# Kernel tuning notes

Hardware: AMD Instinct MI355X
Metric: run time of the kernel (lower is better)

The kernel has to match this reference:

```python
import jax, jax.numpy as jnp
from jax import lax
import numpy as np

VOCAB, EMBED, HIDDEN, BATCH, MAXLEN = 32000, 512, 1024, 64, 64


def setup_inputs() -> dict:
    key = jax.random.key(0)
    ks = jax.random.split(key, 18)
    s = 0.02
    H, E, V = HIDDEN, EMBED, VOCAB
    return {
        "thought": jax.random.normal(ks[0], (BATCH, H), jnp.float32),
        "emb_table": jax.random.normal(ks[1], (V, E), jnp.float32) * s,
        "w_ih0": jax.random.normal(ks[2], (4 * H, E + H), jnp.float32) * s,
        "w_hh0": jax.random.normal(ks[3], (4 * H, H), jnp.float32) * s,
        "b_ih0": jax.random.normal(ks[4], (4 * H,), jnp.float32) * s,
        "b_hh0": jax.random.normal(ks[5], (4 * H,), jnp.float32) * s,
        "w_ih1": jax.random.normal(ks[6], (4 * H, H), jnp.float32) * s,
        "w_hh1": jax.random.normal(ks[7], (4 * H, H), jnp.float32) * s,
        "b_ih1": jax.random.normal(ks[8], (4 * H,), jnp.float32) * s,
        "b_hh1": jax.random.normal(ks[9], (4 * H,), jnp.float32) * s,
        "gw1": jax.random.normal(ks[10], (H, H), jnp.float32) * s,
        "gb1": jax.random.normal(ks[11], (H,), jnp.float32) * s,
        "gw2": jax.random.normal(ks[12], (1, H), jnp.float32) * s,
        "gb2": jax.random.normal(ks[13], (1,), jnp.float32) * s,
        "out_w": jax.random.normal(ks[14], (V, H), jnp.float32) * s,
        "out_b": jax.random.normal(ks[15], (V,), jnp.float32) * s,
        "max_len": MAXLEN,
    }


def lstm_cell(x, h, c, w_ih, w_hh, b_ih, b_hh):
    # torch nn.LSTM gate order: i, f, g, o
    g = x @ w_ih.T + b_ih + h @ w_hh.T + b_hh
    i, f, gg, o = jnp.split(g, 4, axis=-1)
    c2 = jax.nn.sigmoid(f) * c + jax.nn.sigmoid(i) * jnp.tanh(gg)
    return jax.nn.sigmoid(o) * jnp.tanh(c2), c2


def reference(thought, emb_table, w_ih0, w_hh0, b_ih0, b_hh0, w_ih1, w_hh1,
              b_ih1, b_hh1, gw1, gb1, gw2, gb2, out_w, out_b, max_len):
    """Generation branch of BioDecoder.forward (captions=None), eval mode, epoch=0."""
    B, H = thought.shape
    V = out_w.shape[0]
    temperature, top_p, top_k = 0.9, 0.88, 60
    key = jax.random.key(42)
    rows = jnp.arange(B)[:, None]

    def filt(logits):
        # top-k filter
        kth = lax.top_k(logits, top_k)[0][:, -1:]
        logits = jnp.where(logits < kth, -jnp.inf, logits)
        # nucleus (top-p) filter
        sl, si = lax.top_k(logits, V)  # full descending sort
        cum = jnp.cumsum(jax.nn.softmax(sl, axis=-1), axis=-1)
        rm = cum > top_p
        rm = jnp.concatenate([jnp.zeros_like(rm[:, :1]), rm[:, :-1]], axis=-1)  # always keep best
        mask = jnp.zeros_like(rm).at[rows, si].set(rm)
        return jnp.where(mask, -jnp.inf, logits)

    def step(carry, t):
        h1, c1, h2, c2, prev_ctx, word, counts, hist = carry
        x = jnp.concatenate([emb_table[word], prev_ctx], axis=-1)  # [B, E+H]
        h1, c1 = lstm_cell(x, h1, c1, w_ih0, w_hh0, b_ih0, b_hh0)
        h2, c2 = lstm_cell(h1, h2, c2, w_ih1, w_hh1, b_ih1, b_hh1)
        gate = jax.nn.sigmoid(jnp.tanh(h2 @ gw1.T + gb1) @ gw2.T + gb2)  # [B,1]
        out = h2 * gate
        logits = out @ out_w.T + out_b  # [B, V]
        # recency-decayed repetition penalty over full generated history
        ar = jnp.arange(hist.shape[0])
        w = jnp.where(ar < t, 2.5 * jnp.power(0.8, jnp.maximum(t - ar, 0).astype(jnp.float32)), 0.0)
        pen = jnp.zeros((B, V), logits.dtype).at[rows, hist.T].add(
            jnp.broadcast_to(w[None, :], (B, hist.shape[0])))
        # global count penalty (token_counts shared across batch, as in source)
        logits = logits - pen - jnp.where(counts > 1, 2.0 * counts, 0.0)[None, :]
        logits = logits / temperature + (0.3 / (counts + 1.0))[None, :]
        logits = filt(logits)
        nxt = jax.random.categorical(jax.random.fold_in(key, t), logits, axis=-1)  # [B]
        counts = counts.at[nxt].add(1.0)
        hist = hist.at[t].set(nxt)
        return (h1, c1, h2, c2, out, nxt, counts, hist), nxt

    zeros_h = jnp.zeros_like(thought)
    carry0 = (thought, zeros_h, thought, zeros_h, thought,
              jnp.full((B,), 1, jnp.int32),
              jnp.zeros((V,), jnp.float32),
              jnp.zeros((max_len, B), jnp.int32))
    _, tokens = lax.scan(step, carry0, jnp.arange(max_len))
    return tokens.T  # [B, max_len]
```

## Files before the change

kernel.cpp:

```cpp
#include <hip/hip_runtime.h>
#include <stdint.h>
#include <math.h>

#pragma clang fp contract(off)

#define BATCH 64
#define HID   1024
#define EMBD  512
#define VOC   32000
#define G4    4096
#define MAXT  64
#define NTOPK 60
#define CAND_MAX 256

__device__ __forceinline__ float xla_tanh(float x) {
  float ax = fabsf(x);
  float xc = fminf(fmaxf(x, -9.0f), 9.0f);
  float x2 = xc * xc;
  float num = -2.76076847742355e-16f;
  num = fmaf(x2, num, 2.00018790482477e-13f);
  num = fmaf(x2, num, -8.60467152213735e-11f);
  num = fmaf(x2, num, 5.12229709037114e-08f);
  num = fmaf(x2, num, 1.48572235717979e-05f);
  num = fmaf(x2, num, 6.37261928875436e-04f);
  num = fmaf(x2, num, 4.89352455891786e-03f);
  num = xc * num;
  float den = 1.19825839466702e-06f;
  den = fmaf(x2, den, 1.18534705686654e-04f);
  den = fmaf(x2, den, 2.26843463243900e-03f);
  den = fmaf(x2, den, 4.89352518554385e-03f);
  float r = num / den;
  return (ax < 0.0004f) ? x : r;
}

__device__ __forceinline__ float xla_sigmoid(float x) {
  return 0.5f * xla_tanh(0.5f * x) + 0.5f;
}

__device__ __forceinline__ float cephes_expf(float _x) {
  float x = fminf(_x, 88.723164f);
  x = fmaxf(x, -88.723164f);
  float m = floorf(fmaf(x, 1.44269504088896341f, 0.5f));
  float r = fmaf(m, -0.693359375f, x);
  r = fmaf(m, 2.12194440e-4f, r);
  float r2 = r * r;
  float r3 = r2 * r;
  float y, y1, y2;
  y  = fmaf(1.9875691500E-4f, r, 1.3981999507E-3f);
  y1 = fmaf(4.1665795894E-2f, r, 1.6666665459E-1f);
  y2 = r + 1.0f;
  y  = fmaf(y, r, 8.3334519073E-3f);
  y1 = fmaf(y1, r, 5.0000001201E-1f);
  y  = fmaf(y, r3, y1);
  y  = fmaf(y, r2, y2);
  float res = ldexpf(y, (int)m);
  return fmaxf(res, _x);
}

__device__ __forceinline__ float cephes_logf(float _x) {
  float x = fmaxf(_x, 1.17549435e-38f);
  unsigned ux = __float_as_uint(x);
  int e_int = (int)(ux >> 23) - 126;
  x = __uint_as_float((ux & 0x007FFFFFu) | 0x3F000000u);
  float e = (float)e_int;
  if (x < 0.707106781186547524f) { e -= 1.0f; x = x + x - 1.0f; }
  else { x = x - 1.0f; }
  float z = x * x;
  float y = 7.0376836292E-2f;
  y = fmaf(y, x, -1.1514610310E-1f);
  y = fmaf(y, x,  1.1676998740E-1f);
  y = fmaf(y, x, -1.2420140846E-1f);
  y = fmaf(y, x,  1.4249322787E-1f);
  y = fmaf(y, x, -1.6668057665E-1f);
  y = fmaf(y, x,  2.0000714765E-1f);
  y = fmaf(y, x, -2.4999993993E-1f);
  y = fmaf(y, x,  3.3333331174E-1f);
  y = y * x;
  y = y * z;
  y = fmaf(e, -2.12194440e-4f, y);
  y = fmaf(-0.5f, z, y);
  float r = x + y;
  r = fmaf(e, 0.693359375f, r);
  return r;
}

__device__ __forceinline__ unsigned rotl32(unsigned v, int s) {
  return (v << s) | (v >> (32 - s));
}
__device__ __forceinline__ void threefry(unsigned k0, unsigned k1,
                                         unsigned& x0, unsigned& x1) {
  unsigned k2 = k0 ^ k1 ^ 0x1BD11BDAu;
  x0 += k0; x1 += k1;
  x0 += x1; x1 = rotl32(x1, 13); x1 ^= x0;
  x0 += x1; x1 = rotl32(x1, 15); x1 ^= x0;
  x0 += x1; x1 = rotl32(x1, 26); x1 ^= x0;
  x0 += x1; x1 = rotl32(x1,  6); x1 ^= x0;
  x0 += k1; x1 += k2 + 1u;
  x0 += x1; x1 = rotl32(x1, 17); x1 ^= x0;
  x0 += x1; x1 = rotl32(x1, 29); x1 ^= x0;
  x0 += x1; x1 = rotl32(x1, 16); x1 ^= x0;
  x0 += x1; x1 = rotl32(x1, 24); x1 ^= x0;
  x0 += k2; x1 += k0 + 2u;
  x0 += x1; x1 = rotl32(x1, 13); x1 ^= x0;
  x0 += x1; x1 = rotl32(x1, 15); x1 ^= x0;
  x0 += x1; x1 = rotl32(x1, 26); x1 ^= x0;
  x0 += x1; x1 = rotl32(x1,  6); x1 ^= x0;
  x0 += k0; x1 += k1 + 3u;
  x0 += x1; x1 = rotl32(x1, 17); x1 ^= x0;
  x0 += x1; x1 = rotl32(x1, 29); x1 ^= x0;
  x0 += x1; x1 = rotl32(x1, 16); x1 ^= x0;
  x0 += x1; x1 = rotl32(x1, 24); x1 ^= x0;
  x0 += k1; x1 += k2 + 4u;
  x0 += x1; x1 = rotl32(x1, 13); x1 ^= x0;
  x0 += x1; x1 = rotl32(x1, 15); x1 ^= x0;
  x0 += x1; x1 = rotl32(x1, 26); x1 ^= x0;
  x0 += x1; x1 = rotl32(x1,  6); x1 ^= x0;
  x0 += k2; x1 += k0 + 5u;
}

__device__ __forceinline__ float gumbel_val(unsigned k0, unsigned k1, int b, int v) {
  unsigned x0 = 0u, x1 = (unsigned)(b * VOC + v);
  threefry(k0, k1, x0, x1);
  unsigned bits = x0 ^ x1;
  float u = __uint_as_float(0x3f800000u | (bits >> 9)) - 1.0f;
  if (u == 0.0f) u = 1.17549435e-38f;
  return -cephes_logf(-cephes_logf(u));
}

__device__ __forceinline__ unsigned okey(float f) {
  unsigned u = __float_as_uint(f);
  return (u & 0x80000000u) ? ~u : (u | 0x80000000u);
}

__global__ __launch_bounds__(256) void k_init(const float* __restrict__ thought,
    float* h1, float* c1, float* h2, float* c2, float* prev_ctx,
    float* counts, int* word, int* hist) {
  int i = blockIdx.x * blockDim.x + threadIdx.x;
  if (i < BATCH * HID) {
    float tv = thought[i];
    h1[i] = tv; h2[i] = tv; prev_ctx[i] = tv;
    c1[i] = 0.f; c2[i] = 0.f;
  }
  if (i < VOC) counts[i] = 0.f;
  if (i < BATCH) word[i] = 1;
  if (i < MAXT * BATCH) hist[i] = 0;
}

__global__ __launch_bounds__(256) void k_gates0(const float* __restrict__ emb,
    const int* __restrict__ word, const float* __restrict__ prev_ctx,
    const float* __restrict__ h1, const float* __restrict__ w_ih,
    const float* __restrict__ b_ih, const float* __restrict__ w_hh,
    const float* __restrict__ b_hh, float* __restrict__ g) {
  int jl = threadIdx.x & 7, bg = threadIdx.x >> 3;
  int j = blockIdx.x * 8 + jl;
  const float4* wi4 = (const float4*)(w_ih + (size_t)j * (EMBD + HID));
  const float4* wh4 = (const float4*)(w_hh + (size_t)j * HID);
  const float4* e4[2]; const float4* p4[2]; const float4* h4[2];
  #pragma unroll
  for (int i = 0; i < 2; ++i) {
    int b = bg + 32 * i;
    e4[i] = (const float4*)(emb + (size_t)word[b] * EMBD);
    p4[i] = (const float4*)(prev_ctx + (size_t)b * HID);
    h4[i] = (const float4*)(h1 + (size_t)b * HID);
  }
  float acc[2] = {0.f, 0.f};
  float shh[2] = {0.f, 0.f};
  for (int k = 0; k < EMBD / 4; ++k) {
    float4 w = wi4[k];
    #pragma unroll
    for (int i = 0; i < 2; ++i) {
      float4 a = e4[i][k];
      acc[i] = fmaf(a.x, w.x, acc[i]); acc[i] = fmaf(a.y, w.y, acc[i]);
      acc[i] = fmaf(a.z, w.z, acc[i]); acc[i] = fmaf(a.w, w.w, acc[i]);
    }
  }
  for (int k = 0; k < HID / 4; ++k) {
    float4 w = wi4[EMBD / 4 + k];
    #pragma unroll
    for (int i = 0; i < 2; ++i) {
      float4 a = p4[i][k];
      acc[i] = fmaf(a.x, w.x, acc[i]); acc[i] = fmaf(a.y, w.y, acc[i]);
      acc[i] = fmaf(a.z, w.z, acc[i]); acc[i] = fmaf(a.w, w.w, acc[i]);
    }
  }
  for (int k = 0; k < HID / 4; ++k) {
    float4 w = wh4[k];
    #pragma unroll
    for (int i = 0; i < 2; ++i) {
      float4 a = h4[i][k];
      shh[i] = fmaf(a.x, w.x, shh[i]); shh[i] = fmaf(a.y, w.y, shh[i]);
      shh[i] = fmaf(a.z, w.z, shh[i]); shh[i] = fmaf(a.w, w.w, shh[i]);
    }
  }
  float bi = b_ih[j], bh = b_hh[j];
  #pragma unroll
  for (int i = 0; i < 2; ++i) {
    int b = bg + 32 * i;
    g[(size_t)b * G4 + j] = ((acc[i] + bi) + shh[i]) + bh;
  }
}

__global__ __launch_bounds__(256) void k_gates1(const float* __restrict__ xin,
    const float* __restrict__ hin, const float* __restrict__ w_ih,
    const float* __restrict__ b_ih, const float* __restrict__ w_hh,
    const float* __restrict__ b_hh, float* __restrict__ g) {
  int jl = threadIdx.x & 7, bg = threadIdx.x >> 3;
  int j = blockIdx.x * 8 + jl;
  const float4* wi4 = (const float4*)(w_ih + (size_t)j * HID);
  const float4* wh4 = (const float4*)(w_hh + (size_t)j * HID);
  float acc[2] = {0.f, 0.f};
  float shh[2] = {0.f, 0.f};
  for (int k = 0; k < HID / 4; ++k) {
    float4 w = wi4[k];
    #pragma unroll
    for (int i = 0; i < 2; ++i) {
      float4 a = ((const float4*)(xin + (size_t)(bg + 32 * i) * HID))[k];
      acc[i] = fmaf(a.x, w.x, acc[i]); acc[i] = fmaf(a.y, w.y, acc[i]);
      acc[i] = fmaf(a.z, w.z, acc[i]); acc[i] = fmaf(a.w, w.w, acc[i]);
    }
  }
  for (int k = 0; k < HID / 4; ++k) {
    float4 w = wh4[k];
    #pragma unroll
    for (int i = 0; i < 2; ++i) {
      float4 a = ((const float4*)(hin + (size_t)(bg + 32 * i) * HID))[k];
      shh[i] = fmaf(a.x, w.x, shh[i]); shh[i] = fmaf(a.y, w.y, shh[i]);
      shh[i] = fmaf(a.z, w.z, shh[i]); shh[i] = fmaf(a.w, w.w, shh[i]);
    }
  }
  float bi = b_ih[j], bh = b_hh[j];
  #pragma unroll
  for (int i = 0; i < 2; ++i) {
    int b = bg + 32 * i;
    g[(size_t)b * G4 + j] = ((acc[i] + bi) + shh[i]) + bh;
  }
}

__global__ __launch_bounds__(256) void k_cell(const float* __restrict__ g,
    float* __restrict__ h, float* __restrict__ c) {
  int i = blockIdx.x * blockDim.x + threadIdx.x;
  int b = i >> 10, u = i & 1023;
  const float* gb = g + (size_t)b * G4;
  float iv = gb[u], fv = gb[u + 1024], gv = gb[u + 2048], ov = gb[u + 3072];
  float cold = c[i];
  float cnew = xla_sigmoid(fv) * cold + xla_sigmoid(iv) * xla_tanh(gv);
  float hnew = xla_sigmoid(ov) * xla_tanh(cnew);
  c[i] = cnew;
  h[i] = hnew;
}

__global__ __launch_bounds__(256) void k_gtmp(const float* __restrict__ h2,
    const float* __restrict__ gw1, const float* __restrict__ gb1,
    float* __restrict__ gtmp) {
  int ul = threadIdx.x & 3, b = threadIdx.x >> 2;
  int u = blockIdx.x * 4 + ul;
  const float4* w4 = (const float4*)(gw1 + (size_t)u * HID);
  const float4* a4 = (const float4*)(h2 + (size_t)b * HID);
  float acc = 0.f;
  for (int k = 0; k < HID / 4; ++k) {
    float4 w = w4[k];
    float4 a = a4[k];
    acc = fmaf(a.x, w.x, acc); acc = fmaf(a.y, w.y, acc);
    acc = fmaf(a.z, w.z, acc); acc = fmaf(a.w, w.w, acc);
  }
  gtmp[(size_t)b * HID + u] = xla_tanh(acc + gb1[u]);
}

__global__ __launch_bounds__(256) void k_gateout(const float* __restrict__ gtmp,
    const float* __restrict__ gw2, const float* __restrict__ gb2,
    const float* __restrict__ h2, float* __restrict__ prev_ctx) {
  int b = blockIdx.x, tid = threadIdx.x;
  __shared__ float red[256];
  __shared__ float gsh;
  float s = 0.f;
  for (int k = tid; k < HID; k += 256)
    s = fmaf(gtmp[(size_t)b * HID + k], gw2[k], s);
  red[tid] = s;
  __syncthreads();
  for (int st = 128; st > 0; st >>= 1) {
    if (tid < st) red[tid] += red[tid + st];
    __syncthreads();
  }
  if (tid == 0) gsh = xla_sigmoid(red[0] + gb2[0]);
  __syncthreads();
  float gate = gsh;
  for (int k = tid; k < HID; k += 256)
    prev_ctx[(size_t)b * HID + k] = h2[(size_t)b * HID + k] * gate;
}

__global__ __launch_bounds__(256) void k_logits(const float* __restrict__ outp,
    const float* __restrict__ out_w, const float* __restrict__ out_b,
    const float* __restrict__ counts, float* __restrict__ raw,
    float* __restrict__ adj) {
  int vl = threadIdx.x & 63;
  int v = blockIdx.x * 64 + vl;
  int bbase = __builtin_amdgcn_readfirstlane((int)(threadIdx.x >> 6) * 16);
  const float4* w4 = (const float4*)(out_w + (size_t)v * HID);
  const float* ob = outp + (size_t)bbase * HID;
  float acc[16];
  #pragma unroll
  for (int i = 0; i < 16; ++i) acc[i] = 0.f;
  for (int k = 0; k < HID / 4; ++k) {
    float4 w = w4[k];
    #pragma unroll
    for (int i = 0; i < 16; ++i) {
      const float* op = ob + (size_t)i * HID + 4 * (size_t)k;
      acc[i] = fmaf(op[0], w.x, acc[i]);
      acc[i] = fmaf(op[1], w.y, acc[i]);
      acc[i] = fmaf(op[2], w.z, acc[i]);
      acc[i] = fmaf(op[3], w.w, acc[i]);
    }
  }
  float c = counts[v];
  float cpen = (c > 1.0f) ? (2.0f * c) : 0.0f;
  float bonus = 0.3f / (c + 1.0f);
  float bv = out_b[v];
  #pragma unroll
  for (int i = 0; i < 16; ++i) {
    int b = bbase + i;
    float r = acc[i] + bv;
    raw[(size_t)b * VOC + v] = r;
    adj[(size_t)b * VOC + v] = (r - cpen) / 0.9f + bonus;
  }
}

__global__ __launch_bounds__(64) void k_penfix(const int* __restrict__ hist,
    const float* __restrict__ counts, const float* __restrict__ raw,
    float* __restrict__ adj, int t) {
  int b = blockIdx.x, tid = threadIdx.x;
  __shared__ int hcol[MAXT];
  __shared__ float wtab[MAXT];
  if (tid < t) hcol[tid] = hist[tid * BATCH + b];
  wtab[tid] = 2.5f * powf(0.8f, (float)tid);
  __syncthreads();
  int ar = tid;
  if (ar >= t) return;
  int tok = hcol[ar];
  for (int a2 = 0; a2 < ar; ++a2)
    if (hcol[a2] == tok) return;
  float pen = 0.f;
  for (int a2 = ar; a2 < t; ++a2)
    if (hcol[a2] == tok) pen += wtab[t - a2];
  float c = counts[tok];
  float cpen = (c > 1.0f) ? (2.0f * c) : 0.0f;
  float bonus = 0.3f / (c + 1.0f);
  float r = raw[(size_t)b * VOC + tok];
  adj[(size_t)b * VOC + tok] = ((r - pen) - cpen) / 0.9f + bonus;
}

__global__ __launch_bounds__(256) void k_sample(const float* __restrict__ adj,
    float* __restrict__ counts, int* __restrict__ word, int* __restrict__ hist,
    int* __restrict__ out_tokens, int t) {
  int b = blockIdx.x, tid = threadIdx.x;
  const float* row = adj + (size_t)b * VOC;
  __shared__ unsigned bins[256];
  __shared__ unsigned sh_prefix;
  __shared__ int sh_want, sh_cnt;
  __shared__ float cval[CAND_MAX];
  __shared__ int cidx[CAND_MAX];
  __shared__ float sval[CAND_MAX];
  __shared__ int sidx[CAND_MAX];
  __shared__ unsigned char kept[CAND_MAX];
  __shared__ float rval[256];
  __shared__ int ridx[256];
  __shared__ unsigned shk0, shk1;
  if (tid == 0) {
    sh_prefix = 0u; sh_want = NTOPK; sh_cnt = 0;
    unsigned a = 0u, cc = (unsigned)t;
    threefry(0u, 42u, a, cc);
    shk0 = a; shk1 = cc;
  }
  __syncthreads();
  for (int p = 3; p >= 0; --p) {
    bins[tid] = 0u;
    __syncthreads();
    unsigned pref = sh_prefix;
    for (int v = tid; v < VOC; v += 256) {
      unsigned key = okey(row[v]);
      bool match = (p == 3) || (((key ^ pref) >> (8 * (p + 1))) == 0u);
      if (match) atomicAdd(&bins[(key >> (8 * p)) & 255u], 1u);
    }
    __syncthreads();
    if (tid == 0) {
      unsigned cum = 0; int want = sh_want; int sel = 0;
      for (int d = 255; d >= 0; --d) {
        unsigned cd = bins[d];
        if (cum + cd >= (unsigned)want) { sel = d; sh_want = want - (int)cum; break; }
        cum += cd;
      }
      sh_prefix = pref | ((unsigned)sel << (8 * p));
    }
    __syncthreads();
  }
  unsigned kmin = sh_prefix;
  for (int v = tid; v < VOC; v += 256) {
    unsigned key = okey(row[v]);
    if (key >= kmin) {
      int pos = atomicAdd(&sh_cnt, 1);
      if (pos < CAND_MAX) { cval[pos] = row[v]; cidx[pos] = v; }
    }
  }
  __syncthreads();
  int C = sh_cnt; if (C > CAND_MAX) C = CAND_MAX;
  for (int i = tid; i < C; i += 256) {
    float vi = cval[i]; int ii = cidx[i]; int r = 0;
    for (int j = 0; j < C; ++j) {
      float vj = cval[j]; int ij = cidx[j];
      if (vj > vi || (vj == vi && ij < ii)) ++r;
    }
    sval[r] = vi; sidx[r] = ii;
  }
  __syncthreads();
  if (tid == 0) {
    float m = sval[0];
    float psum = 0.f;
    for (int j = 0; j < C; ++j) {
      float p = cephes_expf(sval[j] - m);
      cval[j] = p;
      psum += p;
    }
    float cum = 0.f;
    for (int j = 0; j < C; ++j) {
      kept[j] = (j == 0 || cum <= 0.88f) ? 1 : 0;
      cum += cval[j] / psum;
    }
  }
  __syncthreads();
  float bscore = -INFINITY; int bidx = 0x7FFFFFFF;
  for (int j = tid; j < C; j += 256) {
    if (kept[j]) {
      float gv = gumbel_val(shk0, shk1, b, sidx[j]);
      float sc = gv + sval[j];
      if (sc > bscore || (sc == bscore && sidx[j] < bidx)) { bscore = sc; bidx = sidx[j]; }
    }
  }
  rval[tid] = bscore; ridx[tid] = bidx;
  __syncthreads();
  for (int s = 128; s > 0; s >>= 1) {
    if (tid < s) {
      float ov = rval[tid + s]; int oi = ridx[tid + s];
      if (ov > rval[tid] || (ov == rval[tid] && oi < ridx[tid])) {
        rval[tid] = ov; ridx[tid] = oi;
      }
    }
    __syncthreads();
  }
  if (tid == 0) {
    int tok = ridx[0];
    word[b] = tok;
    hist[t * BATCH + b] = tok;
    out_tokens[b * MAXT + t] = tok;
    atomicAdd(&counts[tok], 1.0f);
  }
}

extern "C" void kernel_launch(void* const* d_in, const int* in_sizes, int n_in,
                              void* d_out, int out_size, void* d_ws, size_t ws_size,
                              hipStream_t stream) {
  const float* thought = (const float*)d_in[0];
  const float* emb     = (const float*)d_in[1];
  const float* w_ih0   = (const float*)d_in[2];
  const float* w_hh0   = (const float*)d_in[3];
  const float* b_ih0   = (const float*)d_in[4];
  const float* b_hh0   = (const float*)d_in[5];
  const float* w_ih1   = (const float*)d_in[6];
  const float* w_hh1   = (const float*)d_in[7];
  const float* b_ih1   = (const float*)d_in[8];
  const float* b_hh1   = (const float*)d_in[9];
  const float* gw1     = (const float*)d_in[10];
  const float* gb1     = (const float*)d_in[11];
  const float* gw2     = (const float*)d_in[12];
  const float* gb2     = (const float*)d_in[13];
  const float* out_w   = (const float*)d_in[14];
  const float* out_b   = (const float*)d_in[15];
  int* out_tokens = (int*)d_out;

  float* F = (float*)d_ws;
  float* h1       = F;
  float* c1       = F + 65536;
  float* h2       = F + 131072;
  float* c2       = F + 196608;
  float* prev_ctx = F + 262144;
  float* gtmp     = F + 327680;
  float* g0       = F + 393216;
  float* g1       = F + 655360;
  float* counts   = F + 917504;
  float* raw      = F + 949504;
  float* adj      = F + 2997504;
  int*   word     = (int*)(F + 5045504);
  int*   hist     = word + 64;

  k_init<<<256, 256, 0, stream>>>(thought, h1, c1, h2, c2, prev_ctx, counts, word, hist);
  for (int t = 0; t < MAXT; ++t) {
    k_gates0<<<512, 256, 0, stream>>>(emb, word, prev_ctx, h1, w_ih0, b_ih0, w_hh0, b_hh0, g0);
    k_cell<<<256, 256, 0, stream>>>(g0, h1, c1);
    k_gates1<<<512, 256, 0, stream>>>(h1, h2, w_ih1, b_ih1, w_hh1, b_hh1, g1);
    k_cell<<<256, 256, 0, stream>>>(g1, h2, c2);
    k_gtmp<<<256, 256, 0, stream>>>(h2, gw1, gb1, gtmp);
    k_gateout<<<64, 256, 0, stream>>>(gtmp, gw2, gb2, h2, prev_ctx);
    k_logits<<<500, 256, 0, stream>>>(prev_ctx, out_w, out_b, counts, raw, adj);
    k_penfix<<<64, 64, 0, stream>>>(hist, counts, raw, adj, t);
    k_sample<<<64, 256, 0, stream>>>(adj, counts, word, hist, out_tokens, t);
  }
}
```

Before: 44.69 ms.

## Fuse penalty fix into sampler, cache radix keys in LDS, widen logits blocks

Merges the repetition-penalty fixup kernel into the sampling kernel, which removes one launch per step. The sampler now reads the logits row from global memory once, turns it into ordered keys held in a 128KB shared array, and reuses those keys for all radix passes and for candidate gathering instead of rereading global memory four times. The logits kernel moves to 512-thread blocks covering 128 vocab entries and loads activations as float4. The large shared allocation limits occupancy of the sampler to one block per CU, and the row being written and read within one kernel depends on the block barrier between the fixup and the scan.

```diff
diff --git a/kernel.cpp b/kernel.cpp
--- a/kernel.cpp
+++ b/kernel.cpp
@@ -131,6 +131,10 @@
   unsigned u = __float_as_uint(f);
   return (u & 0x80000000u) ? ~u : (u | 0x80000000u);
 }
+__device__ __forceinline__ float okey_inv(unsigned key) {
+  unsigned u = (key & 0x80000000u) ? (key & 0x7FFFFFFFu) : ~key;
+  return __uint_as_float(u);
+}
 
 __global__ __launch_bounds__(256) void k_init(const float* __restrict__ thought,
     float* h1, float* c1, float* h2, float* c2, float* prev_ctx,
@@ -288,13 +292,14 @@
     prev_ctx[(size_t)b * HID + k] = h2[(size_t)b * HID + k] * gate;
 }
 
-__global__ __launch_bounds__(256) void k_logits(const float* __restrict__ outp,
+__global__ __launch_bounds__(512) void k_logits(const float* __restrict__ outp,
     const float* __restrict__ out_w, const float* __restrict__ out_b,
     const float* __restrict__ counts, float* __restrict__ raw,
     float* __restrict__ adj) {
-  int vl = threadIdx.x & 63;
-  int v = blockIdx.x * 64 + vl;
-  int bbase = __builtin_amdgcn_readfirstlane((int)(threadIdx.x >> 6) * 16);
+  int lane = threadIdx.x & 63;
+  int wave = threadIdx.x >> 6;
+  int bbase = (wave & 3) * 16;
+  int v = blockIdx.x * 128 + (wave >> 2) * 64 + lane;
   const float4* w4 = (const float4*)(out_w + (size_t)v * HID);
   const float* ob = outp + (size_t)bbase * HID;
   float acc[16];
@@ -304,11 +309,9 @@
     float4 w = w4[k];
     #pragma unroll
     for (int i = 0; i < 16; ++i) {
-      const float* op = ob + (size_t)i * HID + 4 * (size_t)k;
-      acc[i] = fmaf(op[0], w.x, acc[i]);
-      acc[i] = fmaf(op[1], w.y, acc[i]);
-      acc[i] = fmaf(op[2], w.z, acc[i]);
-      acc[i] = fmaf(op[3], w.w, acc[i]);
+      float4 a = ((const float4*)(ob + (size_t)i * HID))[k];
+      acc[i] = fmaf(a.x, w.x, acc[i]); acc[i] = fmaf(a.y, w.y, acc[i]);
+      acc[i] = fmaf(a.z, w.z, acc[i]); acc[i] = fmaf(a.w, w.w, acc[i]);
     }
   }
   float c = counts[v];
@@ -324,35 +327,13 @@
   }
 }
 
-__global__ __launch_bounds__(64) void k_penfix(const int* __restrict__ hist,
-    const float* __restrict__ counts, const float* __restrict__ raw,
-    float* __restrict__ adj, int t) {
-  int b = blockIdx.x, tid = threadIdx.x;
-  __shared__ int hcol[MAXT];
-  __shared__ float wtab[MAXT];
-  if (tid < t) hcol[tid] = hist[tid * BATCH + b];
-  wtab[tid] = 2.5f * powf(0.8f, (float)tid);
-  __syncthreads();
-  int ar = tid;
-  if (ar >= t) return;
-  int tok = hcol[ar];
-  for (int a2 = 0; a2 < ar; ++a2)
-    if (hcol[a2] == tok) return;
-  float pen = 0.f;
-  for (int a2 = ar; a2 < t; ++a2)
-    if (hcol[a2] == tok) pen += wtab[t - a2];
-  float c = counts[tok];
-  float cpen = (c > 1.0f) ? (2.0f * c) : 0.0f;
-  float bonus = 0.3f / (c + 1.0f);
-  float r = raw[(size_t)b * VOC + tok];
-  adj[(size_t)b * VOC + tok] = ((r - pen) - cpen) / 0.9f + bonus;
-}
-
-__global__ __launch_bounds__(256) void k_sample(const float* __restrict__ adj,
+__global__ __launch_bounds__(256) void k_sample(float* __restrict__ adj,
+    const float* __restrict__ raw, const int* __restrict__ hist_in,
     float* __restrict__ counts, int* __restrict__ word, int* __restrict__ hist,
     int* __restrict__ out_tokens, int t) {
   int b = blockIdx.x, tid = threadIdx.x;
-  const float* row = adj + (size_t)b * VOC;
+  float* row = adj + (size_t)b * VOC;
+  __shared__ unsigned keys[VOC];
   __shared__ unsigned bins[256];
   __shared__ unsigned sh_prefix;
   __shared__ int sh_want, sh_cnt;
@@ -364,6 +345,12 @@
   __shared__ float rval[256];
   __shared__ int ridx[256];
   __shared__ unsigned shk0, shk1;
+  __shared__ int hcol[MAXT];
+  __shared__ float wtab[MAXT];
+
+  if (tid < t) hcol[tid] = hist_in[tid * BATCH + b];
+  if (tid < MAXT) wtab[tid] = 2.5f * powf(0.8f, (float)tid);
+  bins[tid] = 0u;
   if (tid == 0) {
     sh_prefix = 0u; sh_want = NTOPK; sh_cnt = 0;
     unsigned a = 0u, cc = (unsigned)t;
@@ -371,14 +358,55 @@
     shk0 = a; shk1 = cc;
   }
   __syncthreads();
-  for (int p = 3; p >= 0; --p) {
+
+  if (tid < t) {
+    int ar = tid;
+    int tok = hcol[ar];
+    bool first = true;
+    for (int a2 = 0; a2 < ar; ++a2)
+      if (hcol[a2] == tok) { first = false; break; }
+    if (first) {
+      float pen = 0.f;
+      for (int a2 = ar; a2 < t; ++a2)
+        if (hcol[a2] == tok) pen += wtab[t - a2];
+      float c = counts[tok];
+      float cpen = (c > 1.0f) ? (2.0f * c) : 0.0f;
+      float bonus = 0.3f / (c + 1.0f);
+      float r = raw[(size_t)b * VOC + tok];
+      row[tok] = ((r - pen) - cpen) / 0.9f + bonus;
+    }
+  }
+  __syncthreads();
+
+  const float4* row4 = (const float4*)row;
+  for (int i = tid; i < VOC / 4; i += 256) {
+    float4 f = row4[i];
+    unsigned k0 = okey(f.x), k1 = okey(f.y), k2 = okey(f.z), k3 = okey(f.w);
+    keys[4 * i]     = k0; keys[4 * i + 1] = k1;
+    keys[4 * i + 2] = k2; keys[4 * i + 3] = k3;
+    atomicAdd(&bins[k0 >> 24], 1u); atomicAdd(&bins[k1 >> 24], 1u);
+    atomicAdd(&bins[k2 >> 24], 1u); atomicAdd(&bins[k3 >> 24], 1u);
+  }
+  __syncthreads();
+  if (tid == 0) {
+    unsigned cum = 0; int want = sh_want; int sel = 0;
+    for (int d = 255; d >= 0; --d) {
+      unsigned cd = bins[d];
+      if (cum + cd >= (unsigned)want) { sel = d; sh_want = want - (int)cum; break; }
+      cum += cd;
+    }
+    sh_prefix = (unsigned)sel << 24;
+  }
+  __syncthreads();
+
+  for (int p = 2; p >= 0; --p) {
     bins[tid] = 0u;
     __syncthreads();
     unsigned pref = sh_prefix;
     for (int v = tid; v < VOC; v += 256) {
-      unsigned key = okey(row[v]);
-      bool match = (p == 3) || (((key ^ pref) >> (8 * (p + 1))) == 0u);
-      if (match) atomicAdd(&bins[(key >> (8 * p)) & 255u], 1u);
+      unsigned key = keys[v];
+      if (((key ^ pref) >> (8 * (p + 1))) == 0u)
+        atomicAdd(&bins[(key >> (8 * p)) & 255u], 1u);
     }
     __syncthreads();
     if (tid == 0) {
@@ -393,15 +421,17 @@
     __syncthreads();
   }
   unsigned kmin = sh_prefix;
+
   for (int v = tid; v < VOC; v += 256) {
-    unsigned key = okey(row[v]);
+    unsigned key = keys[v];
     if (key >= kmin) {
       int pos = atomicAdd(&sh_cnt, 1);
-      if (pos < CAND_MAX) { cval[pos] = row[v]; cidx[pos] = v; }
+      if (pos < CAND_MAX) { cval[pos] = okey_inv(key); cidx[pos] = v; }
     }
   }
   __syncthreads();
   int C = sh_cnt; if (C > CAND_MAX) C = CAND_MAX;
+
   for (int i = tid; i < C; i += 256) {
     float vi = cval[i]; int ii = cidx[i]; int r = 0;
     for (int j = 0; j < C; ++j) {
@@ -411,6 +441,7 @@
     sval[r] = vi; sidx[r] = ii;
   }
   __syncthreads();
+
   if (tid == 0) {
     float m = sval[0];
     float psum = 0.f;
@@ -426,6 +457,7 @@
     }
   }
   __syncthreads();
+
   float bscore = -INFINITY; int bidx = 0x7FFFFFFF;
   for (int j = tid; j < C; j += 256) {
     if (kept[j]) {
@@ -498,8 +530,7 @@
     k_cell<<<256, 256, 0, stream>>>(g1, h2, c2);
     k_gtmp<<<256, 256, 0, stream>>>(h2, gw1, gb1, gtmp);
     k_gateout<<<64, 256, 0, stream>>>(gtmp, gw2, gb2, h2, prev_ctx);
-    k_logits<<<500, 256, 0, stream>>>(prev_ctx, out_w, out_b, counts, raw, adj);
-    k_penfix<<<64, 64, 0, stream>>>(hist, counts, raw, adj, t);
-    k_sample<<<64, 256, 0, stream>>>(adj, counts, word, hist, out_tokens, t);
-  }
-}
+    k_logits<<<250, 512, 0, stream>>>(prev_ctx, out_w, out_b, counts, raw, adj);
+    k_sample<<<64, 256, 0, stream>>>(adj, raw, hist, counts, word, hist, out_tokens, t);
+  }
+}
```

Measured after the change: 55.93 ms. 1.25x slower.
